# Kernel optimization log

Hardware: AMD Instinct MI355X
Metric: run time of the kernel (lower is better)

## Reference

```python
import jax, jax.numpy as jnp
from jax import lax
import numpy as np

B, H, W = 8, 1024, 1024
NUM_POINTS = 10
THRESHOLD_RATIO = 0.5
K_PEAKS = 512  # cap on peak candidates fed to greedy NMS


def setup_inputs() -> dict:
    key = jax.random.key(0)
    ks = jax.random.split(key, 8)
    return {
        "rgb_image": jax.random.uniform(ks[0], (B, 3, H, W), jnp.float32),
        "depth_image": jax.random.uniform(ks[1], (B, 1, H, W), jnp.float32),
        "conv1_w": jax.random.normal(ks[2], (32, 12, 3, 3), jnp.float32) * 0.1,
        "conv1_b": jax.random.normal(ks[3], (32,), jnp.float32) * 0.1,
        "bn_gamma": jnp.ones((32,), jnp.float32),
        "bn_beta": jnp.zeros((32,), jnp.float32),
        "bn_mean": jax.random.normal(ks[4], (32,), jnp.float32) * 0.1,
        "bn_var": jax.random.uniform(ks[5], (32,), jnp.float32) + 0.5,
        "conv2_w": jax.random.normal(ks[6], (1, 32, 1, 1), jnp.float32) * 0.1,
        "conv2_b": jnp.zeros((1,), jnp.float32),
    }


def dwt2(x):
    # Haar DWT exactly as in the torch module (row split then column split)
    x01 = x[..., 0::2, :] * 0.5
    x02 = x[..., 1::2, :] * 0.5
    LL = x01[..., 0::2] + x02[..., 0::2]
    LH = x01[..., 0::2] - x02[..., 0::2]
    HL = x01[..., 1::2] + x02[..., 1::2]
    HH = x01[..., 1::2] - x02[..., 1::2]
    return LL, LH, HL, HH


def conv2d(x, w, b=None, pad=0, groups=1):
    y = lax.conv_general_dilated(x, w, (1, 1), [(pad, pad), (pad, pad)],
                                 dimension_numbers=("NCHW", "OIHW", "NCHW"),
                                 feature_group_count=groups)
    if b is not None:
        y = y + b[None, :, None, None]
    return y


def gaussian_smooth(x, k=5, sigma=1.0):
    ax = jnp.arange(-(k // 2), k // 2 + 1, dtype=jnp.float32)
    xx, yy = jnp.meshgrid(ax, ax, indexing="ij")
    ker = jnp.exp(-(xx ** 2 + yy ** 2) / (2.0 * sigma ** 2))
    ker = ker / ker.sum()
    C = x.shape[1]
    wk = jnp.tile(ker[None, None], (C, 1, 1, 1))  # depthwise
    return conv2d(x, wk, pad=k // 2, groups=C)


def find_points(s):
    """Greedy spatial-NMS peak picking on a single (h,w) saliency map.
    Returns (NUM_POINTS, 2) normalized (x, y) coords."""
    h, w = s.shape
    min_dist = float(max(max(h, w) // 20, 20))
    flat = s.reshape(-1)
    mp = lax.reduce_window(s, -jnp.inf, lax.max, (3, 3), (1, 1), [(1, 1), (1, 1)])
    peak_flat = ((s == mp) & (s > 0)).reshape(-1)
    peak_scores = jnp.where(peak_flat, flat, -jnp.inf)
    top_vals, top_idx = lax.top_k(peak_scores, K_PEAKS)  # sorted desc = torch argsort
    valid = top_vals > -jnp.inf
    px = (top_idx % w).astype(jnp.float32)
    py = (top_idx // w).astype(jnp.float32)
    pc = jnp.stack([px, py], axis=-1)                     # (K,2)
    dist = jnp.sqrt(((pc[:, None, :] - pc[None, :, :]) ** 2).sum(-1))  # (K,K)
    ar = jnp.arange(K_PEAKS)

    def body(i, st):
        avail, sel, cnt = st
        take = avail[i] & valid[i] & (cnt < NUM_POINTS)
        sel = sel.at[i].set(take)
        suppress = (dist[i] < min_dist) & (ar > i)  # nearby[:i+1]=False in torch
        avail = jnp.where(take, avail & (~suppress), avail)
        return avail, sel, cnt + take.astype(jnp.int32)

    _, sel, n_chosen = lax.fori_loop(
        0, K_PEAKS, body,
        (jnp.ones(K_PEAKS, bool), jnp.zeros(K_PEAKS, bool), jnp.int32(0)))

    # compact chosen peak indices (in descending-score order) into first slots
    pos = jnp.cumsum(sel.astype(jnp.int32)) - 1
    scatter_pos = jnp.where(sel, pos, NUM_POINTS)  # out-of-range -> dropped
    buf = jnp.zeros(NUM_POINTS, jnp.int32).at[scatter_pos].set(top_idx, mode="drop")
    # fallback: top saliency excluding all peaks (matches torch fill-up branch)
    fb_scores = jnp.where(peak_flat, -jnp.inf, flat)
    _, fb_idx = lax.top_k(fb_scores, NUM_POINTS)
    slot = jnp.arange(NUM_POINTS)
    fb = fb_idx[jnp.clip(slot - n_chosen, 0, NUM_POINTS - 1)]
    sel_idx = jnp.where(slot < n_chosen, buf, fb)
    cx = (sel_idx % w).astype(jnp.float32) / w
    cy = (sel_idx // w).astype(jnp.float32) / h
    return jnp.stack([cx, cy], axis=-1)


def boxes_from_mask(masks):
    binm = masks[:, 0] > THRESHOLD_RATIO  # (B,H,W)
    Hh, Ww = binm.shape[1], binm.shape[2]
    rows = binm.any(axis=2)
    cols = binm.any(axis=1)
    ri = jnp.arange(Hh)
    ci = jnp.arange(Ww)
    rmin = jnp.min(jnp.where(rows, ri[None, :], Hh), axis=1)
    rmax = jnp.max(jnp.where(rows, ri[None, :], -1), axis=1)
    cmin = jnp.min(jnp.where(cols, ci[None, :], Ww), axis=1)
    cmax = jnp.max(jnp.where(cols, ci[None, :], -1), axis=1)
    has = rows.any(axis=1)
    boxes = jnp.stack([cmin, rmin, cmax, rmax], axis=-1).astype(jnp.float32)
    default = jnp.array([0.0, 0.0, Ww - 1.0, Hh - 1.0], jnp.float32)
    return jnp.where(has[:, None], boxes, default[None, :])


def reference(rgb_image, depth_image, conv1_w, conv1_b, bn_gamma, bn_beta,
              bn_mean, bn_var, conv2_w, conv2_b):
    rgb_gray = rgb_image.mean(axis=1, keepdims=True)
    rLL, rLH, rHL, rHH = dwt2(rgb_gray)
    dLL, dLH, dHL, dHH = dwt2(depth_image)
    E_rgb = jnp.sqrt(rLH ** 2 + rHL ** 2 + rHH ** 2 + 1e-8)
    E_depth = jnp.sqrt(dLH ** 2 + dHL ** 2 + dHH ** 2 + 1e-8)
    E_rgb_s = gaussian_smooth(E_rgb)
    E_depth_s = gaussian_smooth(E_depth)
    freq = jnp.concatenate(
        [rLL, rLH, rHL, rHH, dLL, dLH, dHL, dHH, E_rgb, E_depth, E_rgb_s, E_depth_s],
        axis=1)  # (B,12,H/2,W/2)
    x = conv2d(freq, conv1_w, conv1_b, pad=1)
    inv = lax.rsqrt(bn_var + 1e-5)
    x = bn_gamma[None, :, None, None] * (x - bn_mean[None, :, None, None]) * inv[None, :, None, None] + bn_beta[None, :, None, None]
    x = jax.nn.gelu(x)
    sal = jax.nn.sigmoid(conv2d(x, conv2_w, conv2_b))  # (B,1,H/2,W/2)
    masks = jax.image.resize(sal, (sal.shape[0], 1, H, W), method="bilinear")
    coords = jax.vmap(find_points)(sal[:, 0])          # (B,N,2)
    labels = jnp.ones((sal.shape[0], NUM_POINTS), jnp.int32)
    boxes = boxes_from_mask(masks)                     # (B,4)
    return coords, labels, boxes, masks
```

## Files before the change

### kernel.cpp

```cpp
#include <hip/hip_runtime.h>
#include <math.h>


#define CHW 262144
#define FULLHW 1048576
#define NB1 64
#define NB2 32
#define PROW 514
#define PREC (514*514)

typedef __attribute__((ext_vector_type(8))) short bf16x8;
typedef __attribute__((ext_vector_type(16))) float f32x16;

static __device__ __forceinline__ unsigned short f2bf(float x) {
  unsigned u = __float_as_uint(x);
  u += 0x7FFFu + ((u >> 16) & 1u);
  return (unsigned short)(u >> 16);
}
static __device__ __forceinline__ float bf2f(unsigned short h) {
  return __uint_as_float(((unsigned)h) << 16);
}

static constexpr size_t OFF_SAL   = 0;
static constexpr size_t OFF_THR   = 8388608;
static constexpr size_t OFF_CNT   = OFF_THR + 256;
static constexpr size_t OFF_CAND  = OFF_CNT + 256;
static constexpr size_t OFF_PART  = OFF_CAND + 131072;
static constexpr size_t OFF_APACK = OFF_PART + 32768;
static constexpr size_t OFF_EP    = OFF_APACK + 20480;
static constexpr size_t OFF_PKM   = OFF_EP + 512;
static constexpr size_t OFF_DYN   = OFF_PKM + 2097152;

static constexpr int SDY[9] = {-1,-1,-1, 0,0,0, 1,1,1};
static constexpr int SDX[9] = {-1, 0, 1,-1,0,1,-1,0,1};

__global__ void k_init(unsigned* __restrict__ cnt,
                       const float* __restrict__ w1, const float* __restrict__ b1,
                       const float* __restrict__ gam, const float* __restrict__ bet,
                       const float* __restrict__ mean, const float* __restrict__ var,
                       const float* __restrict__ w2, const float* __restrict__ b2,
                       unsigned short* __restrict__ apack, float* __restrict__ ep) {
  int i = blockIdx.x * 256 + threadIdx.x;
  if (i < 16) cnt[i] = 0;
  if (i < 9216) {
    int e = i & 7, lane = (i >> 3) & 63, frag = i >> 9;
    int s = frag >> 1, hh = frag & 1;
    int co = lane & 31;
    int c = ((lane >> 5) << 3) + e;
    float val = (c < 12) ? w1[co * 108 + c * 9 + s] : 0.0f;
    unsigned short hb = f2bf(val);
    apack[i] = hh ? f2bf(val - bf2f(hb)) : hb;
  }
  if (i < 96) {
    int t = i >> 5, rem = i & 31, kg = rem >> 4, reg = rem & 15;
    int co = (reg & 3) + 8 * (reg >> 2) + 4 * kg;
    float sc = gam[co] * rsqrtf(var[co] + 1e-5f);
    float v = (t == 0) ? sc
            : (t == 1) ? (b1[co] - mean[co]) * sc + bet[co]
                       : w2[co];
    ep[i] = v;
  } else if (i == 96) {
    ep[96] = b2[0];
  }
}

__global__ __launch_bounds__(256) void k_zero(unsigned short* __restrict__ freq2) {
  int i = blockIdx.x * 256 + threadIdx.x;
  int bi = blockIdx.y;
  if (i >= 8208) return;
  int rec = i >> 2, q = i & 3;
  int row, col;
  if (rec < 514)       { row = 0;   col = rec; }
  else if (rec < 1028) { row = 513; col = rec - 514; }
  else if (rec < 1540) { row = rec - 1028 + 1; col = 0; }
  else                 { row = rec - 1540 + 1; col = 513; }
  uint4* p = (uint4*)(freq2 + ((size_t)bi * PREC + (size_t)row * PROW + col) * 32) + q;
  *p = make_uint4(0u, 0u, 0u, 0u);
}

__global__ __launch_bounds__(256) void k_freq(const float* __restrict__ rgb,
                                              const float* __restrict__ dep,
                                              unsigned short* __restrict__ freq2,
                                              float* __restrict__ ebuf, int b0) {
  int t = blockIdx.x * 256 + threadIdx.x;
  int bi = blockIdx.y;
  int b = b0 + bi;
  int xp = t & 255, y = t >> 8;
  const float* base = rgb + (size_t)b * 3 * FULLHW + (size_t)(2 * y) * 1024 + 4 * xp;
  float4 R0 = *(const float4*)(base);
  float4 R1 = *(const float4*)(base + 1024);
  float4 G0 = *(const float4*)(base + FULLHW);
  float4 G1 = *(const float4*)(base + FULLHW + 1024);
  float4 Bl0 = *(const float4*)(base + 2 * FULLHW);
  float4 Bl1 = *(const float4*)(base + 2 * FULLHW + 1024);
  const float* dbase = dep + (size_t)b * FULLHW + (size_t)(2 * y) * 1024 + 4 * xp;
  float4 D0 = *(const float4*)(dbase);
  float4 D1 = *(const float4*)(dbase + 1024);

  float gt[4], gb[4], dt[4], db_[4];
  gt[0] = (R0.x + G0.x + Bl0.x) / 3.0f; gt[1] = (R0.y + G0.y + Bl0.y) / 3.0f;
  gt[2] = (R0.z + G0.z + Bl0.z) / 3.0f; gt[3] = (R0.w + G0.w + Bl0.w) / 3.0f;
  gb[0] = (R1.x + G1.x + Bl1.x) / 3.0f; gb[1] = (R1.y + G1.y + Bl1.y) / 3.0f;
  gb[2] = (R1.z + G1.z + Bl1.z) / 3.0f; gb[3] = (R1.w + G1.w + Bl1.w) / 3.0f;
  dt[0] = D0.x; dt[1] = D0.y; dt[2] = D0.z; dt[3] = D0.w;
  db_[0] = D1.x; db_[1] = D1.y; db_[2] = D1.z; db_[3] = D1.w;

  unsigned short hs[2][16], ls[2][16];
  float er[2], ed[2];
  #pragma unroll
  for (int j = 0; j < 2; ++j) {
    float a = gt[2 * j] * 0.5f, bb = gb[2 * j] * 0.5f;
    float c = gt[2 * j + 1] * 0.5f, d = gb[2 * j + 1] * 0.5f;
    float v[10];
    v[0] = a + bb; v[1] = a - bb; v[2] = c + d; v[3] = c - d;
    float da = dt[2 * j] * 0.5f, db2 = db_[2 * j] * 0.5f;
    float dc = dt[2 * j + 1] * 0.5f, dd = db_[2 * j + 1] * 0.5f;
    v[4] = da + db2; v[5] = da - db2; v[6] = dc + dd; v[7] = dc - dd;
    v[8] = sqrtf(v[1] * v[1] + v[2] * v[2] + v[3] * v[3] + 1e-8f);
    v[9] = sqrtf(v[5] * v[5] + v[6] * v[6] + v[7] * v[7] + 1e-8f);
    er[j] = v[8]; ed[j] = v[9];
    #pragma unroll
    for (int cc = 0; cc < 10; ++cc) {
      unsigned short hb = f2bf(v[cc]);
      hs[j][cc] = hb;
      ls[j][cc] = f2bf(v[cc] - bf2f(hb));
    }
    #pragma unroll
    for (int cc = 10; cc < 16; ++cc) { hs[j][cc] = 0; ls[j][cc] = 0; }
  }
  unsigned short* dst = freq2 +
      ((size_t)bi * PREC + (size_t)(y + 1) * PROW + (2 * xp + 1)) * 32;
  uint4* d4 = (uint4*)dst;
  d4[0] = ((const uint4*)hs[0])[0]; d4[1] = ((const uint4*)hs[0])[1];
  d4[2] = ((const uint4*)ls[0])[0]; d4[3] = ((const uint4*)ls[0])[1];
  d4[4] = ((const uint4*)hs[1])[0]; d4[5] = ((const uint4*)hs[1])[1];
  d4[6] = ((const uint4*)ls[1])[0]; d4[7] = ((const uint4*)ls[1])[1];
  float* eb = ebuf + (size_t)bi * 2 * CHW + (size_t)y * 512 + 2 * xp;
  *(float2*)(eb) = make_float2(er[0], er[1]);
  *(float2*)(eb + CHW) = make_float2(ed[0], ed[1]);
}

__constant__ float GW[25] = {
  0.00296901f, 0.01330621f, 0.02193824f, 0.01330621f, 0.00296901f,
  0.01330621f, 0.05963435f, 0.09832035f, 0.05963435f, 0.01330621f,
  0.02193824f, 0.09832035f, 0.16210276f, 0.09832035f, 0.02193824f,
  0.01330621f, 0.05963435f, 0.09832035f, 0.05963435f, 0.01330621f,
  0.00296901f, 0.01330621f, 0.02193824f, 0.01330621f, 0.00296901f};

__global__ __launch_bounds__(256) void k_smooth(const float* __restrict__ ebuf,
                                                unsigned short* __restrict__ freq2) {
  int t = blockIdx.x * 256 + threadIdx.x;
  int bi = blockIdx.y;
  int x = t & 511, y = t >> 9;
  const float* eb = ebuf + (size_t)bi * 2 * CHW;
  float accv[2];
  #pragma unroll
  for (int ch = 0; ch < 2; ++ch) {
    const float* fin = eb + ch * CHW;
    float acc = 0.0f;
    #pragma unroll
    for (int i = 0; i < 5; ++i) {
      int yy = y + i - 2;
      if (yy < 0 || yy > 511) continue;
      #pragma unroll
      for (int j = 0; j < 5; ++j) {
        int xx = x + j - 2;
        if (xx < 0 || xx > 511) continue;
        acc += GW[i * 5 + j] * fin[yy * 512 + xx];
      }
    }
    accv[ch] = acc;
  }
  unsigned short* px = freq2 +
      ((size_t)bi * PREC + (size_t)(y + 1) * PROW + (x + 1)) * 32;
  unsigned short h0 = f2bf(accv[0]), h1 = f2bf(accv[1]);
  unsigned short l0 = f2bf(accv[0] - bf2f(h0)), l1 = f2bf(accv[1] - bf2f(h1));
  *(unsigned*)(px + 10) = (unsigned)h0 | ((unsigned)h1 << 16);
  *(unsigned*)(px + 26) = (unsigned)l0 | ((unsigned)l1 << 16);
}

__global__ __launch_bounds__(256) void k_conv(const unsigned short* __restrict__ freq2,
    const unsigned short* __restrict__ apack, const float* __restrict__ ep,
    float* __restrict__ sal, int b0) {
  int tid = threadIdx.x;
  int l = tid & 63, wv = tid >> 6;
  int y = blockIdx.y;
  int xw = blockIdx.x * 128 + wv * 32;
  int bi = blockIdx.z;
  int n = l & 31, kg = l >> 5;

  const unsigned short* fb = freq2 + (size_t)bi * PREC * 32;
  const unsigned short* pb0 = fb + ((size_t)(y + 1) * PROW + (xw + n + 1)) * 32 + kg * 8;
  const unsigned short* ab = apack + l * 8;

  f32x16 acc = {};
  #pragma unroll
  for (int s = 0; s < 9; ++s) {
    const int doff = (SDY[s] * PROW + SDX[s]) * 32;
    const unsigned short* pb = pb0 + doff;
    bf16x8 Bh = *(const bf16x8*)(pb);
    bf16x8 Bl = *(const bf16x8*)(pb + 16);
    bf16x8 Ah = *(const bf16x8*)(ab + s * 1024);
    bf16x8 Al = *(const bf16x8*)(ab + s * 1024 + 512);
    acc = __builtin_amdgcn_mfma_f32_32x32x16_bf16(Ah, Bh, acc, 0, 0, 0);
    acc = __builtin_amdgcn_mfma_f32_32x32x16_bf16(Al, Bh, acc, 0, 0, 0);
    acc = __builtin_amdgcn_mfma_f32_32x32x16_bf16(Ah, Bl, acc, 0, 0, 0);
  }

  const float* e0 = ep + kg * 16;
  const float* e1 = ep + 32 + kg * 16;
  const float* e2 = ep + 64 + kg * 16;
  float s2 = 0.0f;
  #pragma unroll
  for (int r = 0; r < 16; ++r) {
    float t = acc[r] * e0[r] + e1[r];
    float z = t * (1.5957691216057308f + 0.07135481283247183f * (t * t));
    s2 += (t / (1.0f + __expf(-z))) * e2[r];
  }
  s2 += __shfl_xor(s2, 32);
  s2 += ep[96];
  float res = 1.0f / (1.0f + __expf(-s2));
  if (l < 32)
    sal[(size_t)(b0 + bi) * CHW + (size_t)y * 512 + xw + n] = res;
}

__global__ __launch_bounds__(256) void k_resize(const float* __restrict__ sal,
                                                float* __restrict__ masks,
                                                int* __restrict__ part) {
  int b = blockIdx.y;
  int blk = blockIdx.x;
  int t = threadIdx.x;
  const float* sp = sal + (size_t)b * CHW;
  float* mp = masks + (size_t)b * FULLHW;
  int mnX = 0x7FFFFFFF, mxX = -1, mnY = 0x7FFFFFFF, mxY = -1;
  int c0 = 4 * t;
  #pragma unroll
  for (int r = 0; r < 4; ++r) {
    int Y = blk * 4 + r;
    int y0 = (Y - 1) >> 1;
    float wy = (Y & 1) ? 0.25f : 0.75f;
    int y0c = y0 < 0 ? 0 : y0, y1c = (y0 + 1 > 511) ? 511 : y0 + 1;
    const float* r0 = sp + y0c * 512;
    const float* r1 = sp + y1c * 512;
    float o[4];
    #pragma unroll
    for (int j = 0; j < 4; ++j) {
      int X = c0 + j;
      int x0 = (X - 1) >> 1;
      float wx = (X & 1) ? 0.25f : 0.75f;
      int x0c = x0 < 0 ? 0 : x0, x1c = (x0 + 1 > 511) ? 511 : x0 + 1;
      float v00 = r0[x0c], v01 = r0[x1c], v10 = r1[x0c], v11 = r1[x1c];
      o[j] = (1.0f - wy) * ((1.0f - wx) * v00 + wx * v01)
           + wy * ((1.0f - wx) * v10 + wx * v11);
      if (o[j] > 0.5f) {
        mnX = min(mnX, X); mxX = max(mxX, X);
        mnY = min(mnY, Y); mxY = max(mxY, Y);
      }
    }
    *(float4*)(mp + (size_t)Y * 1024 + c0) = make_float4(o[0], o[1], o[2], o[3]);
  }
  __shared__ int s0[256], s1[256], s2[256], s3[256];
  s0[t] = mnX; s1[t] = mxX; s2[t] = mnY; s3[t] = mxY;
  __syncthreads();
  for (int off = 128; off > 0; off >>= 1) {
    if (t < off) {
      s0[t] = min(s0[t], s0[t + off]); s1[t] = max(s1[t], s1[t + off]);
      s2[t] = min(s2[t], s2[t + off]); s3[t] = max(s3[t], s3[t + off]);
    }
    __syncthreads();
  }
  if (t == 0) {
    int* pp = part + (b * 256 + blk) * 4;
    pp[0] = s0[0]; pp[1] = s1[0]; pp[2] = s2[0]; pp[3] = s3[0];
  }
}

__global__ __launch_bounds__(256) void k_boxreduce(const int* __restrict__ part,
                                                   float* __restrict__ out) {
  int b = blockIdx.x, t = threadIdx.x;
  const int* pp = part + (b * 256 + t) * 4;
  __shared__ int s0[256], s1[256], s2[256], s3[256];
  s0[t] = pp[0]; s1[t] = pp[1]; s2[t] = pp[2]; s3[t] = pp[3];
  __syncthreads();
  for (int off = 128; off > 0; off >>= 1) {
    if (t < off) {
      s0[t] = min(s0[t], s0[t + off]); s1[t] = max(s1[t], s1[t + off]);
      s2[t] = min(s2[t], s2[t + off]); s3[t] = max(s3[t], s3[t + off]);
    }
    __syncthreads();
  }
  if (t == 0) {
    float x0, y0, x1, y1;
    if (s3[0] < 0) { x0 = 0.0f; y0 = 0.0f; x1 = 1023.0f; y1 = 1023.0f; }
    else { x0 = (float)s0[0]; y0 = (float)s2[0]; x1 = (float)s1[0]; y1 = (float)s3[0]; }
    out[240 + b * 4 + 0] = x0;
    out[240 + b * 4 + 1] = y0;
    out[240 + b * 4 + 2] = x1;
    out[240 + b * 4 + 3] = y1;
  }
}

__global__ __launch_bounds__(256) void k_hist1(const float* __restrict__ sal,
                                               unsigned* __restrict__ h1p,
                                               unsigned char* __restrict__ pkm) {
  __shared__ unsigned sH[4096];
  int b = blockIdx.y, tid = threadIdx.x;
  for (int i = tid; i < 4096; i += 256) sH[i] = 0;
  __syncthreads();
  const float* sp = sal + (size_t)b * CHW;
  int base = blockIdx.x * 4096;
  for (int it = 0; it < 4; ++it) {
    int p = base + it * 1024 + tid * 4;
    int x0 = p & 511, y = p >> 9;
    int ym = (y > 0) ? y - 1 : 0, yp = (y < 511) ? y + 1 : 511;
    const float* r0 = sp + ym * 512;
    const float* r1 = sp + y * 512;
    const float* r2 = sp + yp * 512;
    float4 m0 = *(const float4*)(r0 + x0);
    float4 m1 = *(const float4*)(r1 + x0);
    float4 m2 = *(const float4*)(r2 + x0);
    float l0 = x0 ? r0[x0 - 1] : m0.x;
    float l1 = x0 ? r1[x0 - 1] : m1.x;
    float l2 = x0 ? r2[x0 - 1] : m2.x;
    float q0 = (x0 < 508) ? r0[x0 + 4] : m0.w;
    float q1 = (x0 < 508) ? r1[x0 + 4] : m1.w;
    float q2 = (x0 < 508) ? r2[x0 + 4] : m2.w;
    float a0[6] = {l0, m0.x, m0.y, m0.z, m0.w, q0};
    float a1[6] = {l1, m1.x, m1.y, m1.z, m1.w, q1};
    float a2[6] = {l2, m2.x, m2.y, m2.z, m2.w, q2};
    unsigned pw = 0;
    #pragma unroll
    for (int j = 0; j < 4; ++j) {
      float r0m = fmaxf(fmaxf(a0[j], a0[j + 1]), a0[j + 2]);
      float r1m = fmaxf(fmaxf(a1[j], a1[j + 1]), a1[j + 2]);
      float r2m = fmaxf(fmaxf(a2[j], a2[j + 1]), a2[j + 2]);
      float cmax = fmaxf(fmaxf(r0m, r1m), r2m);
      float sv = a1[j + 1];
      bool pk = (sv > 0.0f) && (sv >= cmax);
      pw |= (pk ? 1u : 0u) << (8 * j);
      unsigned bin = (__float_as_uint(sv) >> 21) & 2047;
      atomicAdd(&sH[(pk ? 0 : 2048) + bin], 1u);
    }
    *(unsigned*)(pkm + (size_t)b * CHW + p) = pw;
  }
  __syncthreads();
  unsigned* dst = h1p + ((size_t)b * NB1 + blockIdx.x) * 4096;
  for (int i = tid; i < 4096; i += 256) dst[i] = sH[i];
}

__global__ __launch_bounds__(256) void k_scan(const unsigned* __restrict__ hp,
                                              int* __restrict__ thr, int level,
                                              int np) {
  int c = blockIdx.x, b = blockIdx.y, t = threadIdx.x;
  __shared__ unsigned sBins[2048];
  __shared__ unsigned sS[256];
  __shared__ int sT;
  unsigned bv[8] = {0, 0, 0, 0, 0, 0, 0, 0};
  for (int p = 0; p < np; ++p) {
    const unsigned* q = hp + ((size_t)(b * np + p)) * 4096 + c * 2048 + t * 8;
    uint4 a = *(const uint4*)(q);
    uint4 d = *(const uint4*)(q + 4);
    bv[0] += a.x; bv[1] += a.y; bv[2] += a.z; bv[3] += a.w;
    bv[4] += d.x; bv[5] += d.y; bv[6] += d.z; bv[7] += d.w;
  }
  unsigned part = 0;
  #pragma unroll
  for (int r = 0; r < 8; ++r) {
    sBins[t * 8 + r] = bv[r];
    part += bv[r];
  }
  sS[t] = part;
  __syncthreads();
  for (int off = 1; off < 256; off <<= 1) {
    unsigned add = (t + off < 256) ? sS[t + off] : 0;
    __syncthreads();
    sS[t] += add;
    __syncthreads();
  }
  int K = (c == 0) ? 512 : 10;
  int* tb = thr + (c * 8 + b) * 4;
  if (level == 1) { K -= tb[1]; if (K < 1) K = 1; }
  if (t == 0) sT = -1;
  __syncthreads();
  if (sS[t] >= (unsigned)K && (t == 255 || sS[t + 1] < (unsigned)K)) sT = t;
  __syncthreads();
  if (t == 0) {
    int T = 0;
    unsigned run = 0;
    if (sT >= 0) {
      int ts = sT;
      run = (ts < 255) ? sS[ts + 1] : 0;
      for (int r = 7; r >= 0; --r) {
        unsigned v = sBins[ts * 8 + r];
        run += v;
        if (run >= (unsigned)K) { T = ts * 8 + r; run -= v; break; }
      }
    } else {
      T = 0;
      run = sS[0] - sBins[0];
    }
    if (level == 0) { tb[0] = T; tb[1] = (int)run; }
    else           { tb[2] = (tb[0] << 11) | T; }
  }
}

__global__ __launch_bounds__(256) void k_hist2(const float* __restrict__ sal,
                                               const unsigned char* __restrict__ pkm,
                                               const int* __restrict__ thr,
                                               unsigned* __restrict__ h2p) {
  __shared__ unsigned sH[4096];
  int b = blockIdx.y, tid = threadIdx.x;
  for (int i = tid; i < 4096; i += 256) sH[i] = 0;
  __syncthreads();
  int t0 = thr[(0 * 8 + b) * 4];
  int t1 = thr[(1 * 8 + b) * 4];
  const float* sp = sal + (size_t)b * CHW;
  const unsigned char* pp = pkm + (size_t)b * CHW;
  int base = blockIdx.x * 8192;
  for (int it = 0; it < 8; ++it) {
    int p = base + it * 1024 + tid * 4;
    float4 s4 = *(const float4*)(sp + p);
    unsigned pk4 = *(const unsigned*)(pp + p);
    float sv[4] = {s4.x, s4.y, s4.z, s4.w};
    #pragma unroll
    for (int j = 0; j < 4; ++j) {
      bool pk = ((pk4 >> (8 * j)) & 255u) != 0;
      unsigned bits = __float_as_uint(sv[j]);
      int tt = pk ? t0 : t1;
      if ((int)(bits >> 21) == tt)
        atomicAdd(&sH[(pk ? 0 : 2048) + ((bits >> 10) & 2047)], 1u);
    }
  }
  __syncthreads();
  unsigned* dst = h2p + ((size_t)b * NB2 + blockIdx.x) * 4096;
  for (int i = tid; i < 4096; i += 256) dst[i] = sH[i];
}

__global__ __launch_bounds__(256) void k_compact(const float* __restrict__ sal,
                                                 const unsigned char* __restrict__ pkm,
                                                 const int* __restrict__ thr,
                                                 unsigned* __restrict__ cnt,
                                                 unsigned long long* __restrict__ cand) {
  int b = blockIdx.y;
  int p = (blockIdx.x * 256 + threadIdx.x) * 4;
  const float* sp = sal + (size_t)b * CHW;
  float4 s4 = *(const float4*)(sp + p);
  unsigned pk4 = *(const unsigned*)(pkm + (size_t)b * CHW + p);
  unsigned q0 = (unsigned)thr[(0 * 8 + b) * 4 + 2];
  unsigned q1 = (unsigned)thr[(1 * 8 + b) * 4 + 2];
  float sv[4] = {s4.x, s4.y, s4.z, s4.w};
  #pragma unroll
  for (int j = 0; j < 4; ++j) {
    bool pk = ((pk4 >> (8 * j)) & 255u) != 0;
    unsigned bits = __float_as_uint(sv[j]);
    unsigned q = pk ? q0 : q1;
    int c = pk ? 0 : 1;
    if ((bits >> 10) >= q) {
      unsigned pos = atomicAdd(&cnt[c * 8 + b], 1u);
      if (pos < 1024)
        cand[((size_t)(c * 8 + b) << 10) + pos] =
            ((unsigned long long)bits << 32) | (unsigned)(~(p + j));
    }
  }
}

__device__ inline void bitonic1024_desc(unsigned long long* sKey) {
  int t = threadIdx.x;
  for (unsigned k = 2; k <= 1024; k <<= 1) {
    for (unsigned j = k >> 1; j > 0; j >>= 1) {
      __syncthreads();
      #pragma unroll
      for (int e = 0; e < 2; ++e) {
        unsigned i = (unsigned)t + (unsigned)e * 512u;
        unsigned l = i ^ j;
        if (l > i) {
          unsigned long long a = sKey[i], bb = sKey[l];
          if (((i & k) == 0) ? (a < bb) : (a > bb)) { sKey[i] = bb; sKey[l] = a; }
        }
      }
    }
  }
  __syncthreads();
}

__global__ __launch_bounds__(512) void k_nms(const unsigned long long* __restrict__ cand,
                                             const unsigned* __restrict__ cnt,
                                             float* __restrict__ out) {
  __shared__ unsigned long long sKey[1024];
  __shared__ unsigned sIdx[512];
  __shared__ int sAvail[512];
  __shared__ int sSel[16];
  int b = blockIdx.x, t = threadIdx.x;
  if (t < 10) out[160 + b * 10 + t] = 1.0f;
  int Cp = (int)cnt[b]; if (Cp > 1024) Cp = 1024;
  const unsigned long long* cp = cand + ((size_t)b << 10);
  sKey[t] = (t < Cp) ? cp[t] : 0ULL;
  sKey[t + 512] = (t + 512 < Cp) ? cp[t + 512] : 0ULL;
  bitonic1024_desc(sKey);
  sIdx[t] = (unsigned)(~sKey[t]);
  int ncand = (Cp < 512) ? Cp : 512;
  sAvail[t] = (t < ncand) ? 1 : 0;
  __syncthreads();
  int nsel = 0;
  for (int i = 0; i < 512 && nsel < 10; ++i) {
    if (sAvail[i] != 0) {
      unsigned pi = sIdx[i];
      int xi = (int)(pi & 511), yi = (int)(pi >> 9);
      if (t > i && sAvail[t]) {
        int dx = (int)(sIdx[t] & 511) - xi;
        int dy = (int)(sIdx[t] >> 9) - yi;
        if (dx * dx + dy * dy < 625) sAvail[t] = 0;
      }
      if (t == 0) sSel[nsel] = (int)pi;
      ++nsel;
      __syncthreads();
    }
  }
  __syncthreads();
  int Cf = (int)cnt[8 + b]; if (Cf > 1024) Cf = 1024;
  const unsigned long long* cf = cand + ((size_t)(8 + b) << 10);
  sKey[t] = (t < Cf) ? cf[t] : 0ULL;
  sKey[t + 512] = (t + 512 < Cf) ? cf[t + 512] : 0ULL;
  bitonic1024_desc(sKey);
  if (t < 10) {
    int fi;
    if (t < nsel) fi = sSel[t];
    else { int r = t - nsel; if (r > 9) r = 9; fi = (int)((unsigned)(~sKey[r])); }
    out[((size_t)b * 10 + t) * 2 + 0] = (float)(fi & 511) * (1.0f / 512.0f);
    out[((size_t)b * 10 + t) * 2 + 1] = (float)(fi >> 9) * (1.0f / 512.0f);
  }
}

extern "C" void kernel_launch(void* const* d_in, const int* in_sizes, int n_in,
                              void* d_out, int out_size, void* d_ws, size_t ws_size,
                              hipStream_t stream) {
  const float* rgb  = (const float*)d_in[0];
  const float* dep  = (const float*)d_in[1];
  const float* w1   = (const float*)d_in[2];
  const float* b1   = (const float*)d_in[3];
  const float* gam  = (const float*)d_in[4];
  const float* bet  = (const float*)d_in[5];
  const float* bmn  = (const float*)d_in[6];
  const float* bvr  = (const float*)d_in[7];
  const float* w2   = (const float*)d_in[8];
  const float* b2   = (const float*)d_in[9];
  float* out = (float*)d_out;
  char* ws = (char*)d_ws;

  float* sal = (float*)(ws + OFF_SAL);
  int* thr = (int*)(ws + OFF_THR);
  unsigned* cnt = (unsigned*)(ws + OFF_CNT);
  unsigned long long* cand = (unsigned long long*)(ws + OFF_CAND);
  int* part = (int*)(ws + OFF_PART);
  unsigned short* apack = (unsigned short*)(ws + OFF_APACK);
  float* ep = (float*)(ws + OFF_EP);
  unsigned char* pkm = (unsigned char*)(ws + OFF_PKM);

  size_t perE = (size_t)2 * CHW * 4;
  size_t perF = (size_t)PREC * 64;
  long long avail = (long long)ws_size - (long long)OFF_DYN;
  int nb = 1;
  if (avail >= (long long)(perE + perF)) {
    long long m = avail / (long long)(perE + perF);
    nb = (m > 8) ? 8 : (int)m;
  }
  float* ebuf = (float*)(ws + OFF_DYN);
  unsigned short* freq2 = (unsigned short*)(ws + OFF_DYN + perE * (size_t)nb);
  unsigned* h1p = (unsigned*)(ws + OFF_DYN);
  unsigned* h2p = (unsigned*)(ws + OFF_DYN + (size_t)8 * NB1 * 4096 * 4);

  k_init<<<40, 256, 0, stream>>>(cnt, w1, b1, gam, bet, bmn, bvr, w2, b2,
                                 apack, ep);
  k_zero<<<dim3(33, nb), 256, 0, stream>>>(freq2);

  for (int b0 = 0; b0 < 8; b0 += nb) {
    int nbc = (8 - b0 < nb) ? (8 - b0) : nb;
    k_freq<<<dim3(512, nbc), 256, 0, stream>>>(rgb, dep, freq2, ebuf, b0);
    k_smooth<<<dim3(1024, nbc), 256, 0, stream>>>(ebuf, freq2);
    k_conv<<<dim3(4, 512, nbc), 256, 0, stream>>>(freq2, apack, ep, sal, b0);
  }

  k_resize<<<dim3(256, 8), 256, 0, stream>>>(sal, out + 272, part);
  k_boxreduce<<<8, 256, 0, stream>>>(part, out);
  k_hist1<<<dim3(NB1, 8), 256, 0, stream>>>(sal, h1p, pkm);
  k_scan<<<dim3(2, 8), 256, 0, stream>>>(h1p, thr, 0, NB1);
  k_hist2<<<dim3(NB2, 8), 256, 0, stream>>>(sal, pkm, thr, h2p);
  k_scan<<<dim3(2, 8), 256, 0, stream>>>(h2p, thr, 1, NB2);
  k_compact<<<dim3(256, 8), 256, 0, stream>>>(sal, pkm, thr, cnt, cand);
  k_nms<<<8, 512, 0, stream>>>(cand, cnt, out);
}
```

Baseline: 581.7 us.

## Split padded freq buffer into two channel planes and prefetch conv operands

The interleaved 32-short-per-pixel layout becomes two planes of 16 shorts each. Plane 0 holds the 8 DWT channels (hi and lo bf16) and plane 1 holds the edge energies plus the smoothed energies. Each k_conv half-wave now reads its own plane, which may improve coalescing, and all nine stencil B operands are loaded up front so the loads can overlap the MFMA chain. k_smooth now re-reads the edge energies and writes a full 32-byte record. That adds a little traffic but removes the partial 4-byte scattered writes and the zero-padding writes in k_freq.

```diff
diff --git a/kernel.cpp b/kernel.cpp
--- a/kernel.cpp
+++ b/kernel.cpp
@@ -68,13 +68,14 @@
   int i = blockIdx.x * 256 + threadIdx.x;
   int bi = blockIdx.y;
   if (i >= 8208) return;
-  int rec = i >> 2, q = i & 3;
+  int q = i & 1, r = (i >> 1) % 2052, pl = (i >> 1) / 2052;
   int row, col;
-  if (rec < 514)       { row = 0;   col = rec; }
-  else if (rec < 1028) { row = 513; col = rec - 514; }
-  else if (rec < 1540) { row = rec - 1028 + 1; col = 0; }
-  else                 { row = rec - 1540 + 1; col = 513; }
-  uint4* p = (uint4*)(freq2 + ((size_t)bi * PREC + (size_t)row * PROW + col) * 32) + q;
+  if (r < 514)        { row = 0;   col = r; }
+  else if (r < 1028)  { row = 513; col = r - 514; }
+  else if (r < 1540)  { row = r - 1028 + 1; col = 0; }
+  else                { row = r - 1540 + 1; col = 513; }
+  size_t off = ((size_t)(bi * 2 + pl) * PREC + (size_t)row * PROW + col) * 16;
+  uint4* p = (uint4*)(freq2 + off) + q;
   *p = make_uint4(0u, 0u, 0u, 0u);
 }
 
@@ -105,36 +106,31 @@
   dt[0] = D0.x; dt[1] = D0.y; dt[2] = D0.z; dt[3] = D0.w;
   db_[0] = D1.x; db_[1] = D1.y; db_[2] = D1.z; db_[3] = D1.w;
 
-  unsigned short hs[2][16], ls[2][16];
+  unsigned short hs[2][8], ls[2][8];
   float er[2], ed[2];
   #pragma unroll
   for (int j = 0; j < 2; ++j) {
     float a = gt[2 * j] * 0.5f, bb = gb[2 * j] * 0.5f;
     float c = gt[2 * j + 1] * 0.5f, d = gb[2 * j + 1] * 0.5f;
-    float v[10];
+    float v[8];
     v[0] = a + bb; v[1] = a - bb; v[2] = c + d; v[3] = c - d;
     float da = dt[2 * j] * 0.5f, db2 = db_[2 * j] * 0.5f;
     float dc = dt[2 * j + 1] * 0.5f, dd = db_[2 * j + 1] * 0.5f;
     v[4] = da + db2; v[5] = da - db2; v[6] = dc + dd; v[7] = dc - dd;
-    v[8] = sqrtf(v[1] * v[1] + v[2] * v[2] + v[3] * v[3] + 1e-8f);
-    v[9] = sqrtf(v[5] * v[5] + v[6] * v[6] + v[7] * v[7] + 1e-8f);
-    er[j] = v[8]; ed[j] = v[9];
+    er[j] = sqrtf(v[1] * v[1] + v[2] * v[2] + v[3] * v[3] + 1e-8f);
+    ed[j] = sqrtf(v[5] * v[5] + v[6] * v[6] + v[7] * v[7] + 1e-8f);
     #pragma unroll
-    for (int cc = 0; cc < 10; ++cc) {
+    for (int cc = 0; cc < 8; ++cc) {
       unsigned short hb = f2bf(v[cc]);
       hs[j][cc] = hb;
       ls[j][cc] = f2bf(v[cc] - bf2f(hb));
     }
-    #pragma unroll
-    for (int cc = 10; cc < 16; ++cc) { hs[j][cc] = 0; ls[j][cc] = 0; }
   }
   unsigned short* dst = freq2 +
-      ((size_t)bi * PREC + (size_t)(y + 1) * PROW + (2 * xp + 1)) * 32;
+      ((size_t)(bi * 2) * PREC + (size_t)(y + 1) * PROW + (2 * xp + 1)) * 16;
   uint4* d4 = (uint4*)dst;
-  d4[0] = ((const uint4*)hs[0])[0]; d4[1] = ((const uint4*)hs[0])[1];
-  d4[2] = ((const uint4*)ls[0])[0]; d4[3] = ((const uint4*)ls[0])[1];
-  d4[4] = ((const uint4*)hs[1])[0]; d4[5] = ((const uint4*)hs[1])[1];
-  d4[6] = ((const uint4*)ls[1])[0]; d4[7] = ((const uint4*)ls[1])[1];
+  d4[0] = ((const uint4*)hs[0])[0]; d4[1] = ((const uint4*)ls[0])[0];
+  d4[2] = ((const uint4*)hs[1])[0]; d4[3] = ((const uint4*)ls[1])[0];
   float* eb = ebuf + (size_t)bi * 2 * CHW + (size_t)y * 512 + 2 * xp;
   *(float2*)(eb) = make_float2(er[0], er[1]);
   *(float2*)(eb + CHW) = make_float2(ed[0], ed[1]);
@@ -171,12 +167,21 @@
     }
     accv[ch] = acc;
   }
+  float erc = eb[t], edc = eb[CHW + t];
+  unsigned short rec[16];
+  float v4[4] = {erc, edc, accv[0], accv[1]};
+  #pragma unroll
+  for (int j = 0; j < 4; ++j) {
+    unsigned short hb = f2bf(v4[j]);
+    rec[j] = hb;
+    rec[8 + j] = f2bf(v4[j] - bf2f(hb));
+  }
+  #pragma unroll
+  for (int j = 4; j < 8; ++j) { rec[j] = 0; rec[8 + j] = 0; }
   unsigned short* px = freq2 +
-      ((size_t)bi * PREC + (size_t)(y + 1) * PROW + (x + 1)) * 32;
-  unsigned short h0 = f2bf(accv[0]), h1 = f2bf(accv[1]);
-  unsigned short l0 = f2bf(accv[0] - bf2f(h0)), l1 = f2bf(accv[1] - bf2f(h1));
-  *(unsigned*)(px + 10) = (unsigned)h0 | ((unsigned)h1 << 16);
-  *(unsigned*)(px + 26) = (unsigned)l0 | ((unsigned)l1 << 16);
+      ((size_t)(bi * 2 + 1) * PREC + (size_t)(y + 1) * PROW + (x + 1)) * 16;
+  ((uint4*)px)[0] = ((const uint4*)rec)[0];
+  ((uint4*)px)[1] = ((const uint4*)rec)[1];
 }
 
 __global__ __launch_bounds__(256) void k_conv(const unsigned short* __restrict__ freq2,
@@ -189,22 +194,26 @@
   int bi = blockIdx.z;
   int n = l & 31, kg = l >> 5;
 
-  const unsigned short* fb = freq2 + (size_t)bi * PREC * 32;
-  const unsigned short* pb0 = fb + ((size_t)(y + 1) * PROW + (xw + n + 1)) * 32 + kg * 8;
+  const unsigned short* pb0 = freq2 +
+      ((size_t)(bi * 2 + kg) * PREC + (size_t)(y + 1) * PROW + (xw + n + 1)) * 16;
   const unsigned short* ab = apack + l * 8;
 
+  bf16x8 Bh[9], Bl[9];
+  #pragma unroll
+  for (int s = 0; s < 9; ++s) {
+    const int doff = (SDY[s] * PROW + SDX[s]) * 16;
+    Bh[s] = *(const bf16x8*)(pb0 + doff);
+    Bl[s] = *(const bf16x8*)(pb0 + doff + 8);
+  }
+
   f32x16 acc = {};
   #pragma unroll
   for (int s = 0; s < 9; ++s) {
-    const int doff = (SDY[s] * PROW + SDX[s]) * 32;
-    const unsigned short* pb = pb0 + doff;
-    bf16x8 Bh = *(const bf16x8*)(pb);
-    bf16x8 Bl = *(const bf16x8*)(pb + 16);
     bf16x8 Ah = *(const bf16x8*)(ab + s * 1024);
     bf16x8 Al = *(const bf16x8*)(ab + s * 1024 + 512);
-    acc = __builtin_amdgcn_mfma_f32_32x32x16_bf16(Ah, Bh, acc, 0, 0, 0);
-    acc = __builtin_amdgcn_mfma_f32_32x32x16_bf16(Al, Bh, acc, 0, 0, 0);
-    acc = __builtin_amdgcn_mfma_f32_32x32x16_bf16(Ah, Bl, acc, 0, 0, 0);
+    acc = __builtin_amdgcn_mfma_f32_32x32x16_bf16(Ah, Bh[s], acc, 0, 0, 0);
+    acc = __builtin_amdgcn_mfma_f32_32x32x16_bf16(Al, Bh[s], acc, 0, 0, 0);
+    acc = __builtin_amdgcn_mfma_f32_32x32x16_bf16(Ah, Bl[s], acc, 0, 0, 0);
   }
 
   const float* e0 = ep + kg * 16;
```

Result: faster. 524.1 us (-9.9%).
